# Kernel tuning notes

Hardware: AMD Instinct MI355X
Metric: run time of the kernel (lower is better)

## Reference

```python
import jax, jax.numpy as jnp
import numpy as np

HIDDEN = 1024
N_HEADS = 16
HEAD_DIM = HIDDEN // N_HEADS  # 64


def setup_inputs() -> dict:
    key = jax.random.key(0)
    ks = jax.random.split(key, 5)
    B, S = 4, 4096
    x = jax.random.normal(ks[0], (B, S, HIDDEN), dtype=jnp.float32)
    scale = 1.0 / np.sqrt(HIDDEN)
    wq = jax.random.normal(ks[1], (HIDDEN, HIDDEN), dtype=jnp.float32) * scale
    wk = jax.random.normal(ks[2], (HIDDEN, HIDDEN), dtype=jnp.float32) * scale
    wv = jax.random.normal(ks[3], (HIDDEN, HIDDEN), dtype=jnp.float32) * scale
    wo = jax.random.normal(ks[4], (HIDDEN, HIDDEN), dtype=jnp.float32) * scale
    return {"x": x, "wq": wq, "wk": wk, "wv": wv, "wo": wo}


def reference(x, wq, wk, wv, wo):
    # Weights stored as (out, in) like torch nn.Linear; y = x @ W^T
    B, S, H = x.shape
    q = (x @ wq.T).reshape(B, S, N_HEADS, HEAD_DIM)
    k = (x @ wk.T).reshape(B, S, N_HEADS, HEAD_DIM)
    v = (x @ wv.T).reshape(B, S, N_HEADS, HEAD_DIM)
    # Faithful to original: no transpose to (B,H,S,D) -> scores are over HEADS
    # attn: (B, S, H_heads, H_heads)
    attn = jnp.einsum("bshd,bsgd->bshg", q, k) / np.sqrt(HEAD_DIM)
    attn = jax.nn.softmax(attn, axis=-1)
    out = jnp.einsum("bshg,bsgd->bshd", attn, v).reshape(B, S, H)
    return out @ wo.T
```

## Files before the change

kernel.cpp:

```cpp
#include <hip/hip_runtime.h>
#include <hip/hip_bf16.h>


typedef __bf16 bf16;
typedef __attribute__((ext_vector_type(8))) __bf16 bf16x8;
typedef __attribute__((ext_vector_type(4))) float floatx4;

#define HIDDEN 1024
#define BM 128
#define BN 128
#define BK 32

__device__ __forceinline__ void async_load16(const bf16* g, bf16* lds) {
    __builtin_amdgcn_global_load_lds(
        (const __attribute__((address_space(1))) void*)g,
        (__attribute__((address_space(3))) void*)lds, 16, 0, 0);
}

__device__ __forceinline__ bf16x8 load8(const bf16* p) {
    return *(const bf16x8*)p;
}
__device__ __forceinline__ bf16x8 load8(const float* p) {
    floatx4 lo = *(const floatx4*)p;
    floatx4 hi = *(const floatx4*)(p + 4);
    bf16x8 r;
#pragma unroll
    for (int i = 0; i < 4; ++i) { r[i] = (bf16)lo[i]; r[i + 4] = (bf16)hi[i]; }
    return r;
}

__global__ __launch_bounds__(256) void cvt_all(
    const float* __restrict__ x,
    const float* __restrict__ wq, const float* __restrict__ wk,
    const float* __restrict__ wv, const float* __restrict__ wo,
    bf16* __restrict__ xb, bf16* __restrict__ wpk, int mh8)
{
    const int per = (HIDDEN * HIDDEN) / 8;
    int i = blockIdx.x * 256 + threadIdx.x;
    if (i < mh8) {
        *(bf16x8*)&xb[(size_t)i * 8] = load8(&x[(size_t)i * 8]);
    } else {
        int j = i - mh8;
        int wsel = j / per;
        int off  = (j - wsel * per) * 8;
        const float* s = wsel == 0 ? wq : wsel == 1 ? wk : wsel == 2 ? wv : wo;
        *(bf16x8*)&wpk[(size_t)j * 8] = load8(&s[off]);
    }
}

template <typename TC>
__global__ __launch_bounds__(256, 2) void gemm_async(
    const bf16* __restrict__ A, const bf16* __restrict__ W,
    TC* __restrict__ C, int M, int N, int K, int lda, int ldc)
{
    __shared__ __align__(16) bf16 sA[BM * BK];
    __shared__ __align__(16) bf16 sB[BN * BK];

    const int tid  = threadIdx.x;
    const int lane = tid & 63;
    const int w    = tid >> 6;
    const int wm   = w >> 1;
    const int wn   = w & 1;
    const int m0   = blockIdx.x * BM;
    const int n0   = blockIdx.y * BN;
    const int col  = lane & 15;
    const int quad = lane >> 4;
    const int swz  = (quad ^ ((col >> 1) & 3)) * 8;

    floatx4 acc[4][4] = {};

    for (int kt = 0; kt < K; kt += BK) {
#pragma unroll
        for (int i = 0; i < 2; ++i) {
            const int c0  = i * 256 + w * 64;
            const int c   = c0 + lane;
            const int row = c >> 2;
            const int kc  = (c & 3) ^ ((row >> 1) & 3);
            async_load16(&A[(size_t)(m0 + row) * lda + kt + kc * 8], &sA[c0 * 8]);
            async_load16(&W[(size_t)(n0 + row) * K   + kt + kc * 8], &sB[c0 * 8]);
        }
        __syncthreads();

        bf16x8 af[4], bfr[4];
#pragma unroll
        for (int mi = 0; mi < 4; ++mi)
            af[mi] = *(const bf16x8*)&sA[(wm * 64 + mi * 16 + col) * BK + swz];
#pragma unroll
        for (int ni = 0; ni < 4; ++ni)
            bfr[ni] = *(const bf16x8*)&sB[(wn * 64 + ni * 16 + col) * BK + swz];

#pragma unroll
        for (int mi = 0; mi < 4; ++mi)
#pragma unroll
            for (int ni = 0; ni < 4; ++ni)
                acc[mi][ni] = __builtin_amdgcn_mfma_f32_16x16x32_bf16(
                    af[mi], bfr[ni], acc[mi][ni], 0, 0, 0);
        __syncthreads();
    }

#pragma unroll
    for (int mi = 0; mi < 4; ++mi) {
#pragma unroll
        for (int r = 0; r < 4; ++r) {
            const int row = m0 + wm * 64 + mi * 16 + quad * 4 + r;
#pragma unroll
            for (int ni = 0; ni < 4; ++ni) {
                const int cc = n0 + wn * 64 + ni * 16 + col;
                C[(size_t)row * ldc + cc] = (TC)acc[mi][ni][r];
            }
        }
    }
}

template <typename TA, typename TB, typename TC>
__global__ __launch_bounds__(256, 2) void gemm_bt(
    const TA* __restrict__ A, const TB* __restrict__ W,
    TC* __restrict__ C, int M, int N, int K)
{
    __shared__ __align__(16) bf16 sA[BM * BK];
    __shared__ __align__(16) bf16 sB[BN * BK];

    const int tid  = threadIdx.x;
    const int lane = tid & 63;
    const int w    = tid >> 6;
    const int wm   = w >> 1;
    const int wn   = w & 1;
    const int m0   = blockIdx.x * BM;
    const int n0   = blockIdx.y * BN;
    const int col  = lane & 15;
    const int quad = lane >> 4;

    floatx4 acc[4][4] = {};

    for (int kt = 0; kt < K; kt += BK) {
        bf16x8 ga[2], gb[2];
#pragma unroll
        for (int i = 0; i < 2; ++i) {
            const int c   = i * 256 + tid;
            const int row = c >> 2;
            const int kc  = c & 3;
            ga[i] = load8(&A[(size_t)(m0 + row) * K + kt + kc * 8]);
            gb[i] = load8(&W[(size_t)(n0 + row) * K + kt + kc * 8]);
        }
        __syncthreads();
#pragma unroll
        for (int i = 0; i < 2; ++i) {
            const int c = i * 256 + tid;
            *(bf16x8*)&sA[c * 8] = ga[i];
            *(bf16x8*)&sB[c * 8] = gb[i];
        }
        __syncthreads();

        bf16x8 af[4], bfr[4];
#pragma unroll
        for (int mi = 0; mi < 4; ++mi)
            af[mi] = *(const bf16x8*)&sA[(wm * 64 + mi * 16 + col) * BK + quad * 8];
#pragma unroll
        for (int ni = 0; ni < 4; ++ni)
            bfr[ni] = *(const bf16x8*)&sB[(wn * 64 + ni * 16 + col) * BK + quad * 8];

#pragma unroll
        for (int mi = 0; mi < 4; ++mi)
#pragma unroll
            for (int ni = 0; ni < 4; ++ni)
                acc[mi][ni] = __builtin_amdgcn_mfma_f32_16x16x32_bf16(
                    af[mi], bfr[ni], acc[mi][ni], 0, 0, 0);
    }

#pragma unroll
    for (int mi = 0; mi < 4; ++mi) {
#pragma unroll
        for (int r = 0; r < 4; ++r) {
            const int row = m0 + wm * 64 + mi * 16 + quad * 4 + r;
#pragma unroll
            for (int ni = 0; ni < 4; ++ni) {
                const int cc = n0 + wn * 64 + ni * 16 + col;
                C[(size_t)row * N + cc] = (TC)acc[mi][ni][r];
            }
        }
    }
}

__global__ __launch_bounds__(256) void attn_heads(
    bf16* base, size_t koff, size_t voff, int stride, bf16* ob)
{
    __shared__ __align__(16) bf16 sP[4][16 * 40];
    __shared__ __align__(16) bf16 sVt[4][64 * 40];

    const int tid   = threadIdx.x;
    const int lane  = tid & 63;
    const int w     = tid >> 6;
    const int token = blockIdx.x * 4 + w;
    const int col   = lane & 15;
    const int quad  = lane >> 4;

    bf16* qt = base + (size_t)token * stride;
    const bf16* kt = qt + koff;
    const bf16* vt = qt + voff;
    bf16* ot = ob + (size_t)token * HIDDEN;

    const bf16x8 z = {};
    *(bf16x8*)&sVt[w][lane * 40 + 16] = z;
    *(bf16x8*)&sVt[w][lane * 40 + 24] = z;
    if (lane < 16) {
        *(bf16x8*)&sP[w][lane * 40 + 16] = z;
        *(bf16x8*)&sP[w][lane * 40 + 24] = z;
    }

    bf16x8 qa0 = *(const bf16x8*)&qt[col * 64 + quad * 8];
    bf16x8 qa1 = *(const bf16x8*)&qt[col * 64 + 32 + quad * 8];
    bf16x8 kb0 = *(const bf16x8*)&kt[col * 64 + quad * 8];
    bf16x8 kb1 = *(const bf16x8*)&kt[col * 64 + 32 + quad * 8];
    floatx4 s = {};
    s = __builtin_amdgcn_mfma_f32_16x16x32_bf16(qa0, kb0, s, 0, 0, 0);
    s = __builtin_amdgcn_mfma_f32_16x16x32_bf16(qa1, kb1, s, 0, 0, 0);

    bf16x8 vc0, vc1;
#pragma unroll
    for (int j = 0; j < 8; ++j)  vc0[j] = vt[j * 64 + lane];
#pragma unroll
    for (int j = 0; j < 8; ++j)  vc1[j] = vt[(j + 8) * 64 + lane];
    *(bf16x8*)&sVt[w][lane * 40]     = vc0;
    *(bf16x8*)&sVt[w][lane * 40 + 8] = vc1;

#pragma unroll
    for (int r = 0; r < 4; ++r) {
        float x = s[r] * 0.125f;
        float m = x;
#pragma unroll
        for (int off = 1; off < 16; off <<= 1)
            m = fmaxf(m, __shfl_xor(m, off));
        float e = __expf(x - m);
        float su = e;
#pragma unroll
        for (int off = 1; off < 16; off <<= 1)
            su += __shfl_xor(su, off);
        sP[w][(quad * 4 + r) * 40 + col] = (bf16)(e / su);
    }

    bf16x8 pa = *(const bf16x8*)&sP[w][col * 40 + quad * 8];
#pragma unroll
    for (int dt = 0; dt < 4; ++dt) {
        bf16x8 vb = *(const bf16x8*)&sVt[w][(dt * 16 + col) * 40 + quad * 8];
        floatx4 o4 = {};
        o4 = __builtin_amdgcn_mfma_f32_16x16x32_bf16(pa, vb, o4, 0, 0, 0);
#pragma unroll
        for (int r = 0; r < 4; ++r)
            ot[(quad * 4 + r) * 64 + dt * 16 + col] = (bf16)o4[r];
    }
}

extern "C" void kernel_launch(void* const* d_in, const int* in_sizes, int n_in,
                              void* d_out, int out_size, void* d_ws, size_t ws_size,
                              hipStream_t stream) {
    const float* x  = (const float*)d_in[0];
    const float* wq = (const float*)d_in[1];
    const float* wk = (const float*)d_in[2];
    const float* wv = (const float*)d_in[3];
    const float* wo = (const float*)d_in[4];
    float* out = (float*)d_out;

    const int M = in_sizes[0] / HIDDEN;
    const size_t MH = (size_t)M * HIDDEN;
    const size_t WH = (size_t)HIDDEN * HIDDEN;

    const size_t need = (MH + 4 * WH + (size_t)M * 3 * HIDDEN) * sizeof(bf16);

    if (ws_size >= need) {
        bf16* xb  = (bf16*)d_ws;
        bf16* wpk = xb + MH;
        bf16* qkv = wpk + 4 * WH;

        const int mh8 = (int)(MH / 8);
        const int nchunks = mh8 + (int)(4 * WH / 8);
        cvt_all<<<dim3(nchunks / 256), 256, 0, stream>>>(x, wq, wk, wv, wo,
                                                         xb, wpk, mh8);

        gemm_async<bf16><<<dim3(M / BM, 3 * HIDDEN / BN), 256, 0, stream>>>(
            xb, wpk, qkv, M, 3 * HIDDEN, HIDDEN, HIDDEN, 3 * HIDDEN);

        attn_heads<<<dim3(M / 4), 256, 0, stream>>>(qkv, 1024, 2048,
                                                    3 * HIDDEN, xb);

        gemm_async<float><<<dim3(M / BM, HIDDEN / BN), 256, 0, stream>>>(
            xb, wpk + 3 * WH, out, M, HIDDEN, HIDDEN, HIDDEN, HIDDEN);
    } else {
        bf16* qb = (bf16*)d_ws;
        bf16* kb = qb + MH;
        bf16* vb = kb + MH;
        dim3 grid(M / BM, HIDDEN / BN), block(256);
        gemm_bt<float, float, bf16><<<grid, block, 0, stream>>>(x, wq, qb, M, HIDDEN, HIDDEN);
        gemm_bt<float, float, bf16><<<grid, block, 0, stream>>>(x, wk, kb, M, HIDDEN, HIDDEN);
        gemm_bt<float, float, bf16><<<grid, block, 0, stream>>>(x, wv, vb, M, HIDDEN, HIDDEN);
        attn_heads<<<dim3(M / 4), block, 0, stream>>>(qb, MH, 2 * MH, HIDDEN, qb);
        gemm_bt<bf16, float, float><<<grid, block, 0, stream>>>(qb, wo, out, M, HIDDEN, HIDDEN);
    }
}
```

Baseline: 311.8 us.

## Replace GEMM with 256x256 8-wave double-buffered pipelined kernel

```diff
diff --git a/kernel.cpp b/kernel.cpp
--- a/kernel.cpp
+++ b/kernel.cpp
@@ -10,6 +10,15 @@
 #define BM 128
 #define BN 128
 #define BK 32
+
+#define FENCE() asm volatile("" ::: "memory")
+#define BAR()                                                                  \
+    do {                                                                       \
+        FENCE();                                                               \
+        __builtin_amdgcn_s_barrier();                                          \
+        FENCE();                                                               \
+    } while (0)
+#define VMCNT(N) asm volatile("s_waitcnt vmcnt(" #N ")" ::: "memory")
 
 __device__ __forceinline__ void async_load16(const bf16* g, bf16* lds) {
     __builtin_amdgcn_global_load_lds(
@@ -48,10 +57,154 @@
     }
 }
 
+
+template <int S>
+__device__ __forceinline__ void stage_half(const bf16* __restrict__ gbase,
+                                           int ld, int kt, bf16* lhalf,
+                                           int h, int tid) {
+#pragma unroll
+    for (int j = 0; j < 2; ++j) {
+        const int ci = j * 512 + tid;
+        const int rr = ci >> 3;
+        const int cs = (ci & 7) ^ (rr & 7);
+        const int gr = h * S + (rr & (S - 1)) + (rr >> (S == 64 ? 6 : 5)) * (2 * S);
+        async_load16(&gbase[(size_t)gr * ld + kt + cs * 8], &lhalf[ci * 8]);
+    }
+}
+
+__device__ __forceinline__ void ld_a4(const bf16* h, int wm, int col, int quad,
+                                      int cx, bf16x8* a) {
+#pragma unroll
+    for (int i = 0; i < 4; ++i) {
+        const int rr = i * 16 + col + (wm << 6);
+#pragma unroll
+        for (int kk = 0; kk < 2; ++kk)
+            a[i * 2 + kk] =
+                *(const bf16x8*)&h[rr * 64 + (((kk << 2) + quad) ^ cx) * 8];
+    }
+}
+__device__ __forceinline__ void ld_b2(const bf16* h, int wn, int col, int quad,
+                                      int cx, bf16x8* b) {
+#pragma unroll
+    for (int j = 0; j < 2; ++j) {
+        const int rr = j * 16 + col + (wn << 5);
+#pragma unroll
+        for (int kk = 0; kk < 2; ++kk)
+            b[j * 2 + kk] =
+                *(const bf16x8*)&h[rr * 64 + (((kk << 2) + quad) ^ cx) * 8];
+    }
+}
+
+template <int H, int G>
+__device__ __forceinline__ void mmq(floatx4 (&acc)[8][4], const bf16x8 (&a)[8],
+                                    const bf16x8 (&bb)[4]) {
+    __builtin_amdgcn_s_setprio(1);
+#pragma unroll
+    for (int i = 0; i < 4; ++i)
+#pragma unroll
+        for (int j = 0; j < 2; ++j)
+#pragma unroll
+            for (int kk = 0; kk < 2; ++kk)
+                acc[H * 4 + i][G * 2 + j] =
+                    __builtin_amdgcn_mfma_f32_16x16x32_bf16(
+                        a[i * 2 + kk], bb[j * 2 + kk],
+                        acc[H * 4 + i][G * 2 + j], 0, 0, 0);
+    __builtin_amdgcn_s_setprio(0);
+}
+
 template <typename TC>
-__global__ __launch_bounds__(256, 2) void gemm_async(
+__global__ __launch_bounds__(512, 2) void gemm8p(
     const bf16* __restrict__ A, const bf16* __restrict__ W,
-    TC* __restrict__ C, int M, int N, int K, int lda, int ldc)
+    TC* __restrict__ C, int K, int lda, int ldc)
+{
+    __shared__ __align__(16) bf16 sA[2][2][128 * 64];
+    __shared__ __align__(16) bf16 sB[2][2][128 * 64];
+
+    const int tid  = threadIdx.x;
+    const int lane = tid & 63;
+    const int w    = tid >> 6;
+    const int wm   = w >> 2;
+    const int wn   = w & 3;
+    const int m0   = blockIdx.x * 256;
+    const int n0   = blockIdx.y * 256;
+    const int col  = lane & 15;
+    const int quad = lane >> 4;
+    const int cx   = col & 7;
+
+    const bf16* Ab = A + (size_t)m0 * lda;
+    const bf16* Wb = W + (size_t)n0 * K;
+
+    floatx4 acc[8][4] = {};
+    bf16x8 a[8], b0[4], b1[4];
+
+    const int T = K / 64;
+
+    stage_half<64>(Ab, lda, 0, sA[0][0], 0, tid);
+    stage_half<32>(Wb, K,   0, sB[0][0], 0, tid);
+    stage_half<32>(Wb, K,   0, sB[0][1], 1, tid);
+    stage_half<64>(Ab, lda, 0, sA[0][1], 1, tid);
+    if (T > 1) {
+        stage_half<64>(Ab, lda, 64, sA[1][0], 0, tid);
+        stage_half<32>(Wb, K,   64, sB[1][0], 0, tid);
+        stage_half<32>(Wb, K,   64, sB[1][1], 1, tid);
+        VMCNT(6);
+    } else {
+        VMCNT(0);
+    }
+    BAR();
+
+    for (int t = 0; t < T; ++t) {
+        const int b   = t & 1;
+        const int kt1 = (t + 1) * 64;
+        const int kt2 = (t + 2) * 64;
+
+        ld_a4(sA[b][0], wm, col, quad, cx, a);
+        ld_b2(sB[b][0], wn, col, quad, cx, b0);
+        if (t + 1 < T) stage_half<64>(Ab, lda, kt1, sA[b ^ 1][1], 1, tid);
+        VMCNT(8);
+        BAR();
+        mmq<0, 0>(acc, a, b0);
+        BAR();
+
+        ld_b2(sB[b][1], wn, col, quad, cx, b1);
+        if (t + 2 < T) stage_half<64>(Ab, lda, kt2, sA[b][0], 0, tid);
+        VMCNT(8);
+        BAR();
+        mmq<0, 1>(acc, a, b1);
+        BAR();
+
+        ld_a4(sA[b][1], wm, col, quad, cx, a);
+        if (t + 2 < T) stage_half<32>(Wb, K, kt2, sB[b][0], 0, tid);
+        VMCNT(8);
+        BAR();
+        mmq<1, 1>(acc, a, b1);
+        BAR();
+
+        if (t + 2 < T) stage_half<32>(Wb, K, kt2, sB[b][1], 1, tid);
+        VMCNT(8);
+        BAR();
+        mmq<1, 0>(acc, a, b0);
+        BAR();
+    }
+
+#pragma unroll
+    for (int mi = 0; mi < 8; ++mi) {
+#pragma unroll
+        for (int r = 0; r < 4; ++r) {
+            const int row = m0 + wm * 128 + mi * 16 + quad * 4 + r;
+#pragma unroll
+            for (int ni = 0; ni < 4; ++ni) {
+                const int cc = n0 + wn * 64 + ni * 16 + col;
+                C[(size_t)row * ldc + cc] = (TC)acc[mi][ni][r];
+            }
+        }
+    }
+}
+
+template <typename TA, typename TB, typename TC>
+__global__ __launch_bounds__(256, 2) void gemm_bt(
+    const TA* __restrict__ A, const TB* __restrict__ W,
+    TC* __restrict__ C, int M, int N, int K)
 {
     __shared__ __align__(16) bf16 sA[BM * BK];
     __shared__ __align__(16) bf16 sB[BN * BK];
@@ -65,70 +218,6 @@
     const int n0   = blockIdx.y * BN;
     const int col  = lane & 15;
     const int quad = lane >> 4;
-    const int swz  = (quad ^ ((col >> 1) & 3)) * 8;
-
-    floatx4 acc[4][4] = {};
-
-    for (int kt = 0; kt < K; kt += BK) {
-#pragma unroll
-        for (int i = 0; i < 2; ++i) {
-            const int c0  = i * 256 + w * 64;
-            const int c   = c0 + lane;
-            const int row = c >> 2;
-            const int kc  = (c & 3) ^ ((row >> 1) & 3);
-            async_load16(&A[(size_t)(m0 + row) * lda + kt + kc * 8], &sA[c0 * 8]);
-            async_load16(&W[(size_t)(n0 + row) * K   + kt + kc * 8], &sB[c0 * 8]);
-        }
-        __syncthreads();
-
-        bf16x8 af[4], bfr[4];
-#pragma unroll
-        for (int mi = 0; mi < 4; ++mi)
-            af[mi] = *(const bf16x8*)&sA[(wm * 64 + mi * 16 + col) * BK + swz];
-#pragma unroll
-        for (int ni = 0; ni < 4; ++ni)
-            bfr[ni] = *(const bf16x8*)&sB[(wn * 64 + ni * 16 + col) * BK + swz];
-
-#pragma unroll
-        for (int mi = 0; mi < 4; ++mi)
-#pragma unroll
-            for (int ni = 0; ni < 4; ++ni)
-                acc[mi][ni] = __builtin_amdgcn_mfma_f32_16x16x32_bf16(
-                    af[mi], bfr[ni], acc[mi][ni], 0, 0, 0);
-        __syncthreads();
-    }
-
-#pragma unroll
-    for (int mi = 0; mi < 4; ++mi) {
-#pragma unroll
-        for (int r = 0; r < 4; ++r) {
-            const int row = m0 + wm * 64 + mi * 16 + quad * 4 + r;
-#pragma unroll
-            for (int ni = 0; ni < 4; ++ni) {
-                const int cc = n0 + wn * 64 + ni * 16 + col;
-                C[(size_t)row * ldc + cc] = (TC)acc[mi][ni][r];
-            }
-        }
-    }
-}
-
-template <typename TA, typename TB, typename TC>
-__global__ __launch_bounds__(256, 2) void gemm_bt(
-    const TA* __restrict__ A, const TB* __restrict__ W,
-    TC* __restrict__ C, int M, int N, int K)
-{
-    __shared__ __align__(16) bf16 sA[BM * BK];
-    __shared__ __align__(16) bf16 sB[BN * BK];
-
-    const int tid  = threadIdx.x;
-    const int lane = tid & 63;
-    const int w    = tid >> 6;
-    const int wm   = w >> 1;
-    const int wn   = w & 1;
-    const int m0   = blockIdx.x * BM;
-    const int n0   = blockIdx.y * BN;
-    const int col  = lane & 15;
-    const int quad = lane >> 4;
 
     floatx4 acc[4][4] = {};
 
@@ -266,7 +355,7 @@
 
     const size_t need = (MH + 4 * WH + (size_t)M * 3 * HIDDEN) * sizeof(bf16);
 
-    if (ws_size >= need) {
+    if (ws_size >= need && (M % 256) == 0) {
         bf16* xb  = (bf16*)d_ws;
         bf16* wpk = xb + MH;
         bf16* qkv = wpk + 4 * WH;
@@ -276,14 +365,14 @@
         cvt_all<<<dim3(nchunks / 256), 256, 0, stream>>>(x, wq, wk, wv, wo,
                                                          xb, wpk, mh8);
 
-        gemm_async<bf16><<<dim3(M / BM, 3 * HIDDEN / BN), 256, 0, stream>>>(
-            xb, wpk, qkv, M, 3 * HIDDEN, HIDDEN, HIDDEN, 3 * HIDDEN);
+        gemm8p<bf16><<<dim3(M / 256, 3 * HIDDEN / 256), 512, 0, stream>>>(
+            xb, wpk, qkv, HIDDEN, HIDDEN, 3 * HIDDEN);
 
         attn_heads<<<dim3(M / 4), 256, 0, stream>>>(qkv, 1024, 2048,
                                                     3 * HIDDEN, xb);
 
-        gemm_async<float><<<dim3(M / BM, HIDDEN / BN), 256, 0, stream>>>(
-            xb, wpk + 3 * WH, out, M, HIDDEN, HIDDEN, HIDDEN, HIDDEN);
+        gemm8p<float><<<dim3(M / 256, HIDDEN / 256), 512, 0, stream>>>(
+            xb, wpk + 3 * WH, out, HIDDEN, HIDDEN, HIDDEN);
     } else {
         bf16* qb = (bf16*)d_ws;
         bf16* kb = qb + MH;
```

Result: faster. 288.5 us (-7.5%).
